# Optimization experiments

Measured on AMD Instinct MI355X. Metric: run time of the kernel, lower is better.

The kernel has to match this reference:

```python
import jax, jax.numpy as jnp
import numpy as np

N_NODES = 50000
N_EDGES = 800000
D_IN = 128
D_OUT = 128


def setup_inputs() -> dict:
    key = jax.random.key(0)
    k1, k2, k3, k4, k5 = jax.random.split(key, 5)
    x = jax.random.normal(k1, (N_NODES, D_IN), dtype=jnp.float32)
    edge_index = jax.random.randint(k2, (2, N_EDGES), 0, N_NODES, dtype=jnp.int64)
    scale = 1.0 / np.sqrt(D_IN)
    W_rel = jax.random.normal(k3, (D_OUT, D_IN), dtype=jnp.float32) * scale
    b_rel = jax.random.normal(k4, (D_OUT,), dtype=jnp.float32) * scale
    W_root = jax.random.normal(k5, (D_OUT, D_IN), dtype=jnp.float32) * scale
    return {"x": x, "edge_index": edge_index, "W_rel": W_rel, "b_rel": b_rel, "W_root": W_root}


def reference(x, edge_index, W_rel, b_rel, W_root):
    # PyG GraphConv (aggr='add'):
    #   out_i = W_rel @ (sum_{j->i} x_j) + b_rel + W_root @ x_i
    # followed by ReLU (normalization=None, dropout=0 -> identity).
    src = edge_index[0]  # message source j
    dst = edge_index[1]  # message target i
    n = x.shape[0]
    agg = jax.ops.segment_sum(x[src], dst, num_segments=n)  # [N, D_IN]
    out = agg @ W_rel.T + b_rel + x @ W_root.T              # [N, D_OUT]
    return jax.nn.relu(out)
```

## Files before the change

kernel.cpp:

```cpp
#include <hip/hip_runtime.h>
#include <hip/hip_bf16.h>


#define N_NODES 50000
#define N_EDGES 800000
#define D 128
#define SLOTS 48
#define NPB 32
#define KC 32
#define SROW 136

#define CVT_N  (N_NODES * (D / 2))
#define PACK_N (8 * 8 * 64 * 8)

typedef __attribute__((ext_vector_type(8))) short short8;
typedef __attribute__((ext_vector_type(4))) float floatx4;

__device__ __forceinline__ float bf2f(unsigned short u) {
    return __uint_as_float((unsigned int)u << 16);
}
__device__ __forceinline__ unsigned short f2bf(float f) {
    __hip_bfloat16 h = __float2bfloat16(f);
    return *(unsigned short*)&h;
}

__device__ __forceinline__ int wave_detect_i64(const int* __restrict__ ei) {
    int lane = threadIdx.x & 63;
    int v = ei[2 * lane + 1];
    return __ballot(v == 0) == ~0ull;
}

__global__ __launch_bounds__(256) void zero_f4_kernel(float4* __restrict__ p, int n4) {
    int i = blockIdx.x * 256 + threadIdx.x;
    if (i < n4) p[i] = make_float4(0.f, 0.f, 0.f, 0.f);
}

__global__ void detect_kernel(const int* __restrict__ ei, int* __restrict__ flag) {
    if (threadIdx.x == 0 && blockIdx.x == 0) {
        int any = 0;
        for (int i = 0; i < 64; ++i) any |= ei[2 * i + 1];
        flag[0] = (any == 0) ? 1 : 0;
    }
}

__global__ __launch_bounds__(256) void prep_kernel(const float2* __restrict__ x2,
                                                   ushort2* __restrict__ xb2,
                                                   const float* __restrict__ Wrel,
                                                   const float* __restrict__ Wroot,
                                                   unsigned short* __restrict__ pwc,
                                                   int* __restrict__ cnt) {
    int i = blockIdx.x * 256 + threadIdx.x;
    if (i < CVT_N) {
        float2 f = x2[i];
        xb2[i] = make_ushort2(f2bf(f.x), f2bf(f.y));
    } else if (i < CVT_N + PACK_N) {
        int idx  = i - CVT_N;
        int j    = idx & 7;
        int lane = (idx >> 3) & 63;
        int n0   = (idx >> 9) & 7;
        int t    = idx >> 12;
        int n = n0 * 16 + (lane & 15);
        int k = t * 32 + (lane >> 4) * 8 + j;
        float w = (k < D) ? Wrel[n * D + k] : Wroot[n * D + (k - D)];
        pwc[idx] = f2bf(w);
    } else if (i < CVT_N + PACK_N + N_NODES + 4) {
        cnt[i - CVT_N - PACK_N] = 0;
    }
}

__global__ __launch_bounds__(256) void append_kernel(const int* __restrict__ ei,
                                                     int* __restrict__ cnt,
                                                     int* __restrict__ slots,
                                                     int* __restrict__ ovf_cnt,
                                                     int* __restrict__ ovf) {
    int i64 = wave_detect_i64(ei);
    int base = (blockIdx.x * 256 + threadIdx.x) * 4;
    if (base >= N_EDGES) return;
    int s0, s1, s2, s3, d0, d1, d2, d3;
    if (i64) {
        int4 a = *(const int4*)&ei[2 * base];
        int4 b = *(const int4*)&ei[2 * base + 4];
        s0 = a.x; s1 = a.z; s2 = b.x; s3 = b.z;
        int4 c = *(const int4*)&ei[2 * N_EDGES + 2 * base];
        int4 e = *(const int4*)&ei[2 * N_EDGES + 2 * base + 4];
        d0 = c.x; d1 = c.z; d2 = e.x; d3 = e.z;
    } else {
        int4 sv = *(const int4*)&ei[base];
        int4 dv = *(const int4*)&ei[N_EDGES + base];
        s0 = sv.x; s1 = sv.y; s2 = sv.z; s3 = sv.w;
        d0 = dv.x; d1 = dv.y; d2 = dv.z; d3 = dv.w;
    }
    bool v0 = (unsigned)s0 < N_NODES && (unsigned)d0 < N_NODES;
    bool v1 = (unsigned)s1 < N_NODES && (unsigned)d1 < N_NODES;
    bool v2 = (unsigned)s2 < N_NODES && (unsigned)d2 < N_NODES;
    bool v3 = (unsigned)s3 < N_NODES && (unsigned)d3 < N_NODES;
    int p0 = v0 ? atomicAdd(&cnt[d0], 1) : 0;
    int p1 = v1 ? atomicAdd(&cnt[d1], 1) : 0;
    int p2 = v2 ? atomicAdd(&cnt[d2], 1) : 0;
    int p3 = v3 ? atomicAdd(&cnt[d3], 1) : 0;
    if (v0) { if (p0 < SLOTS) slots[d0 * SLOTS + p0] = s0;
              else { int o = atomicAdd(ovf_cnt, 1); ovf[2 * o] = d0; ovf[2 * o + 1] = s0; } }
    if (v1) { if (p1 < SLOTS) slots[d1 * SLOTS + p1] = s1;
              else { int o = atomicAdd(ovf_cnt, 1); ovf[2 * o] = d1; ovf[2 * o + 1] = s1; } }
    if (v2) { if (p2 < SLOTS) slots[d2 * SLOTS + p2] = s2;
              else { int o = atomicAdd(ovf_cnt, 1); ovf[2 * o] = d2; ovf[2 * o + 1] = s2; } }
    if (v3) { if (p3 < SLOTS) slots[d3 * SLOTS + p3] = s3;
              else { int o = atomicAdd(ovf_cnt, 1); ovf[2 * o] = d3; ovf[2 * o + 1] = s3; } }
}

__global__ __launch_bounds__(256) void GraphConvLayer_55783035240593_kernel(
        const ushort2* __restrict__ xb2,
        const unsigned short* __restrict__ xb,
        const int* __restrict__ cnt,
        const int* __restrict__ slots,
        const int* __restrict__ ovf_cnt,
        const int* __restrict__ ovf,
        const unsigned short* __restrict__ pwc,
        const float* __restrict__ b_rel,
        float* __restrict__ out) {
    __shared__ unsigned short sA[16 * SROW];
    int wid  = threadIdx.x >> 6;
    int lane = threadIdx.x & 63;
    int node0 = blockIdx.x * 16;
    int tov = ovf_cnt[0];

    for (int li = 0; li < 4; ++li) {
        int node = node0 + wid * 4 + li;
        int kk = cnt[node];
        if (kk > SLOTS) kk = SLOTS;
        int myidx = (lane < kk) ? slots[node * SLOTS + lane] : 0;
        float ax = 0.f, ay = 0.f;
        for (int j = 0; j < kk; j += 8) {
            int s0 = __shfl(myidx, j);
            int s1 = __shfl(myidx, j + 1);
            int s2 = __shfl(myidx, j + 2);
            int s3 = __shfl(myidx, j + 3);
            int s4 = __shfl(myidx, j + 4);
            int s5 = __shfl(myidx, j + 5);
            int s6 = __shfl(myidx, j + 6);
            int s7 = __shfl(myidx, j + 7);
            ushort2 u0 = xb2[(size_t)s0 * (D / 2) + lane];
            ushort2 u1 = xb2[(size_t)s1 * (D / 2) + lane];
            ushort2 u2 = xb2[(size_t)s2 * (D / 2) + lane];
            ushort2 u3 = xb2[(size_t)s3 * (D / 2) + lane];
            ushort2 u4 = xb2[(size_t)s4 * (D / 2) + lane];
            ushort2 u5 = xb2[(size_t)s5 * (D / 2) + lane];
            ushort2 u6 = xb2[(size_t)s6 * (D / 2) + lane];
            ushort2 u7 = xb2[(size_t)s7 * (D / 2) + lane];
            float m1 = (j + 1 < kk) ? 1.f : 0.f;
            float m2 = (j + 2 < kk) ? 1.f : 0.f;
            float m3 = (j + 3 < kk) ? 1.f : 0.f;
            float m4 = (j + 4 < kk) ? 1.f : 0.f;
            float m5 = (j + 5 < kk) ? 1.f : 0.f;
            float m6 = (j + 6 < kk) ? 1.f : 0.f;
            float m7 = (j + 7 < kk) ? 1.f : 0.f;
            ax += bf2f(u0.x) + m1 * bf2f(u1.x) + m2 * bf2f(u2.x) + m3 * bf2f(u3.x)
                + m4 * bf2f(u4.x) + m5 * bf2f(u5.x) + m6 * bf2f(u6.x) + m7 * bf2f(u7.x);
            ay += bf2f(u0.y) + m1 * bf2f(u1.y) + m2 * bf2f(u2.y) + m3 * bf2f(u3.y)
                + m4 * bf2f(u4.y) + m5 * bf2f(u5.y) + m6 * bf2f(u6.y) + m7 * bf2f(u7.y);
        }
        if (tov > 0) {
            for (int t2 = 0; t2 < tov; ++t2) {
                if (ovf[2 * t2] == node) {
                    ushort2 u = xb2[(size_t)ovf[2 * t2 + 1] * (D / 2) + lane];
                    ax += bf2f(u.x);
                    ay += bf2f(u.y);
                }
            }
        }
        *(ushort2*)&sA[(wid * 4 + li) * SROW + 2 * lane] =
            make_ushort2(f2bf(ax), f2bf(ay));
    }
    __syncthreads();

    int m = lane & 15, quad = lane >> 4;
    const unsigned short* arow = &sA[m * SROW + quad * 8];
    const unsigned short* xrow = xb + (size_t)(node0 + m) * D + quad * 8;

    floatx4 acc0 = (floatx4){0.f, 0.f, 0.f, 0.f};
    floatx4 acc1 = (floatx4){0.f, 0.f, 0.f, 0.f};
#pragma unroll
    for (int t = 0; t < 8; ++t) {
        short8 afrag = (t < 4) ? *(const short8*)(arow + t * 32)
                               : *(const short8*)(xrow + (t - 4) * 32);
        const unsigned short* bb = pwc + ((size_t)(t * 8 + wid * 2) * 64 + lane) * 8;
        short8 b0 = *(const short8*)bb;
        short8 b1 = *(const short8*)(bb + 64 * 8);
        acc0 = __builtin_amdgcn_mfma_f32_16x16x32_bf16(afrag, b0, acc0, 0, 0, 0);
        acc1 = __builtin_amdgcn_mfma_f32_16x16x32_bf16(afrag, b1, acc1, 0, 0, 0);
    }

#pragma unroll
    for (int q = 0; q < 2; ++q) {
        floatx4 a = q ? acc1 : acc0;
        int n = (wid * 2 + q) * 16 + m;
        float bias = b_rel[n];
#pragma unroll
        for (int r = 0; r < 4; ++r) {
            int node = node0 + quad * 4 + r;
            out[(size_t)node * D + n] = fmaxf(a[r] + bias, 0.f);
        }
    }
}

__global__ __launch_bounds__(256) void pack_w_kernel(const float* __restrict__ W,
                                                     float* __restrict__ pw) {
    int idx = blockIdx.x * 256 + threadIdx.x;
    if (idx >= D * D) return;
    int o = idx >> 7, k = idx & 127;
    pw[k * D + o] = W[o * D + k];
}

__global__ __launch_bounds__(256) void hist_kernel(const int* __restrict__ ei,
                                                   int* __restrict__ deg) {
    int i64 = wave_detect_i64(ei);
    int base = (blockIdx.x * 256 + threadIdx.x) * 4;
    if (base >= N_EDGES) return;
    int d0, d1, d2, d3;
    if (i64) {
        int4 a = *(const int4*)&ei[2 * N_EDGES + 2 * base];
        int4 b = *(const int4*)&ei[2 * N_EDGES + 2 * base + 4];
        d0 = a.x; d1 = a.z; d2 = b.x; d3 = b.z;
    } else {
        int4 v = *(const int4*)&ei[N_EDGES + base];
        d0 = v.x; d1 = v.y; d2 = v.z; d3 = v.w;
    }
    if ((unsigned)d0 < N_NODES) atomicAdd(&deg[d0], 1);
    if ((unsigned)d1 < N_NODES) atomicAdd(&deg[d1], 1);
    if ((unsigned)d2 < N_NODES) atomicAdd(&deg[d2], 1);
    if ((unsigned)d3 < N_NODES) atomicAdd(&deg[d3], 1);
}

__device__ __forceinline__ int wave_iscan(int v, int lane) {
#pragma unroll
    for (int off = 1; off < 64; off <<= 1) {
        int u = __shfl_up(v, off, 64);
        if (lane >= off) v += u;
    }
    return v;
}

__global__ __launch_bounds__(1024) void scan_kernel(const int* __restrict__ deg,
                                                    int* __restrict__ offsets,
                                                    int* __restrict__ cursor) {
    __shared__ int wsum[16];
    __shared__ int base_s;
    int t = threadIdx.x, lane = t & 63, w = t >> 6;
    if (t == 0) { base_s = 0; offsets[0] = 0; }
    __syncthreads();
    for (int c0 = 0; c0 < N_NODES; c0 += 1024) {
        int idx = c0 + t;
        int v = (idx < N_NODES) ? deg[idx] : 0;
        int inc = wave_iscan(v, lane);
        if (lane == 63) wsum[w] = inc;
        __syncthreads();
        if (w == 0) {
            int s = (lane < 16) ? wsum[lane] : 0;
            int si = wave_iscan(s, lane);
            if (lane < 16) wsum[lane] = si - s;
        }
        __syncthreads();
        int tot = base_s + wsum[w] + inc;
        if (idx < N_NODES) {
            offsets[idx + 1] = tot;
            cursor[idx] = tot - v;
        }
        __syncthreads();
        if (t == 1023) base_s = tot;
        __syncthreads();
    }
}

__global__ __launch_bounds__(256) void reorder_kernel(const int* __restrict__ ei,
                                                      int* __restrict__ cursor,
                                                      int* __restrict__ csr_src) {
    int i64 = wave_detect_i64(ei);
    int base = (blockIdx.x * 256 + threadIdx.x) * 4;
    if (base >= N_EDGES) return;
    int s0, s1, s2, s3, d0, d1, d2, d3;
    if (i64) {
        int4 a = *(const int4*)&ei[2 * base];
        int4 b = *(const int4*)&ei[2 * base + 4];
        s0 = a.x; s1 = a.z; s2 = b.x; s3 = b.z;
        int4 c = *(const int4*)&ei[2 * N_EDGES + 2 * base];
        int4 e = *(const int4*)&ei[2 * N_EDGES + 2 * base + 4];
        d0 = c.x; d1 = c.z; d2 = e.x; d3 = e.z;
    } else {
        int4 sv = *(const int4*)&ei[base];
        int4 dv = *(const int4*)&ei[N_EDGES + base];
        s0 = sv.x; s1 = sv.y; s2 = sv.z; s3 = sv.w;
        d0 = dv.x; d1 = dv.y; d2 = dv.z; d3 = dv.w;
    }
    bool v0 = (unsigned)s0 < N_NODES && (unsigned)d0 < N_NODES;
    bool v1 = (unsigned)s1 < N_NODES && (unsigned)d1 < N_NODES;
    bool v2 = (unsigned)s2 < N_NODES && (unsigned)d2 < N_NODES;
    bool v3 = (unsigned)s3 < N_NODES && (unsigned)d3 < N_NODES;
    int p0 = v0 ? atomicAdd(&cursor[d0], 1) : 0;
    int p1 = v1 ? atomicAdd(&cursor[d1], 1) : 0;
    int p2 = v2 ? atomicAdd(&cursor[d2], 1) : 0;
    int p3 = v3 ? atomicAdd(&cursor[d3], 1) : 0;
    if (v0) csr_src[p0] = s0;
    if (v1) csr_src[p1] = s1;
    if (v2) csr_src[p2] = s2;
    if (v3) csr_src[p3] = s3;
}

__global__ __launch_bounds__(256) void gather_kernel(const float2* __restrict__ x2,
                                                     const int* __restrict__ csr_src,
                                                     const int* __restrict__ offsets,
                                                     float2* __restrict__ agg2) {
    int node = blockIdx.x * 4 + (threadIdx.x >> 6);
    int lane = threadIdx.x & 63;
    if (node >= N_NODES) return;
    int beg = offsets[node], end = offsets[node + 1];
    float2 acc = make_float2(0.f, 0.f);
    for (int e = beg; e < end; ++e) {
        int s = csr_src[e];
        float2 f = x2[(size_t)s * (D / 2) + lane];
        acc.x += f.x;
        acc.y += f.y;
    }
    agg2[(size_t)node * (D / 2) + lane] = acc;
}

__global__ __launch_bounds__(256) void scatter_kernel(const float2* __restrict__ x2,
                                                      const int* __restrict__ ei,
                                                      const int* __restrict__ flag,
                                                      float* __restrict__ agg) {
    int wave = threadIdx.x >> 6;
    int lane = threadIdx.x & 63;
    int e = blockIdx.x * 4 + wave;
    if (e >= N_EDGES) return;
    int i64 = flag ? flag[0] : 0;
    int s, d;
    if (i64) { s = ei[2 * e]; d = ei[2 * N_EDGES + 2 * e]; }
    else     { s = ei[e];     d = ei[N_EDGES + e]; }
    if ((unsigned)s >= N_NODES || (unsigned)d >= N_NODES) return;
    float2 f = x2[(size_t)s * (D / 2) + lane];
    atomicAdd(&agg[(size_t)d * D + 2 * lane + 0], f.x);
    atomicAdd(&agg[(size_t)d * D + 2 * lane + 1], f.y);
}

__global__ __launch_bounds__(256) void gemm_f32_kernel(
        const float2* __restrict__ x2,
        const float* __restrict__ pwrel,
        const float* __restrict__ pwroot,
        const float* __restrict__ b_rel,
        float* __restrict__ out) {
    __shared__ float sWrel[KC * D];
    __shared__ float sWroot[KC * D];
    __shared__ float2 sAm[NPB * (KC / 2)];
    __shared__ float2 sXm[NPB * (KC / 2)];

    int t = threadIdx.x;
    int node0 = blockIdx.x * NPB;
    int tn = t >> 5;
    int to = t & 31;

    float acc[4][4];
#pragma unroll
    for (int a = 0; a < 4; ++a)
#pragma unroll
        for (int b = 0; b < 4; ++b) acc[a][b] = 0.0f;

    for (int c = 0; c < 4; ++c) {
        __syncthreads();
#pragma unroll
        for (int r = 0; r < 4; ++r) {
            int i = r * 256 + t;
            ((float4*)sWrel)[i]  = ((const float4*)(pwrel  + c * KC * D))[i];
            ((float4*)sWroot)[i] = ((const float4*)(pwroot + c * KC * D))[i];
        }
#pragma unroll
        for (int r = 0; r < 2; ++r) {
            int i = r * 256 + t;
            int n = i >> 4, k2 = i & 15;
            int node = node0 + n;
            float2 av = make_float2(0.f, 0.f), xv = make_float2(0.f, 0.f);
            if (node < N_NODES) {
                av = ((const float2*)out)[(size_t)node * (D / 2) + c * (KC / 2) + k2];
                xv = x2[(size_t)node * (D / 2) + c * (KC / 2) + k2];
            }
            sAm[i] = av;
            sXm[i] = xv;
        }
        __syncthreads();

#pragma unroll
        for (int k2 = 0; k2 < KC / 2; ++k2) {
            float4 wr0 = *(const float4*)&sWrel[(2 * k2 + 0) * D + to * 4];
            float4 wr1 = *(const float4*)&sWrel[(2 * k2 + 1) * D + to * 4];
            float4 wt0 = *(const float4*)&sWroot[(2 * k2 + 0) * D + to * 4];
            float4 wt1 = *(const float4*)&sWroot[(2 * k2 + 1) * D + to * 4];
#pragma unroll
            for (int ni = 0; ni < 4; ++ni) {
                float2 a  = sAm[(tn * 4 + ni) * (KC / 2) + k2];
                float2 xx = sXm[(tn * 4 + ni) * (KC / 2) + k2];
                acc[ni][0] += a.x * wr0.x + a.y * wr1.x + xx.x * wt0.x + xx.y * wt1.x;
                acc[ni][1] += a.x * wr0.y + a.y * wr1.y + xx.x * wt0.y + xx.y * wt1.y;
                acc[ni][2] += a.x * wr0.z + a.y * wr1.z + xx.x * wt0.z + xx.y * wt1.z;
                acc[ni][3] += a.x * wr0.w + a.y * wr1.w + xx.x * wt0.w + xx.y * wt1.w;
            }
        }
    }

    int o0 = to * 4;
    float4 bias = *(const float4*)&b_rel[o0];
#pragma unroll
    for (int ni = 0; ni < 4; ++ni) {
        int node = node0 + tn * 4 + ni;
        if (node >= N_NODES) continue;
        float4 v;
        v.x = fmaxf(acc[ni][0] + bias.x, 0.f);
        v.y = fmaxf(acc[ni][1] + bias.y, 0.f);
        v.z = fmaxf(acc[ni][2] + bias.z, 0.f);
        v.w = fmaxf(acc[ni][3] + bias.w, 0.f);
        *(float4*)&out[(size_t)node * D + o0] = v;
    }
}

__global__ __launch_bounds__(128) void gemm_fallback_kernel(const float* __restrict__ x,
                                                            const float* __restrict__ Wrel,
                                                            const float* __restrict__ Wroot,
                                                            const float* __restrict__ b_rel,
                                                            float* __restrict__ out) {
    __shared__ float rowA[D];
    __shared__ float rowX[D];
    int node = blockIdx.x;
    int o = threadIdx.x;
    rowA[o] = out[(size_t)node * D + o];
    rowX[o] = x[(size_t)node * D + o];
    __syncthreads();
    float acc = b_rel[o];
    const float4* wr = (const float4*)&Wrel[o * D];
    const float4* wt = (const float4*)&Wroot[o * D];
#pragma unroll 8
    for (int k4 = 0; k4 < D / 4; ++k4) {
        float4 w = wr[k4], u = wt[k4];
        const float* a = &rowA[k4 * 4];
        const float* xx = &rowX[k4 * 4];
        acc += a[0] * w.x + a[1] * w.y + a[2] * w.z + a[3] * w.w
             + xx[0] * u.x + xx[1] * u.y + xx[2] * u.z + xx[3] * u.w;
    }
    __syncthreads();
    out[(size_t)node * D + o] = fmaxf(acc, 0.f);
}

extern "C" void kernel_launch(void* const* d_in, const int* in_sizes, int n_in,
                              void* d_out, int out_size, void* d_ws, size_t ws_size,
                              hipStream_t stream) {
    const float* x      = (const float*)d_in[0];
    const int*   ei     = (const int*)d_in[1];
    const float* W_rel  = (const float*)d_in[2];
    const float* b_rel  = (const float*)d_in[3];
    const float* W_root = (const float*)d_in[4];
    float*       out    = (float*)d_out;

    char* p = (char*)d_ws;
    size_t o0 = 16;
    int*            flag    = (int*)p;
    unsigned short* pwc     = (unsigned short*)(p + o0);  o0 += (size_t)PACK_N * 2;
    unsigned short* xb      = (unsigned short*)(p + o0);  o0 += (size_t)N_NODES * D * 2;
    int*            cnt     = (int*)(p + o0);             o0 += (size_t)N_NODES * 4;
    int*            ovf_cnt = (int*)(p + o0);             o0 += 16;
    int*            slots   = (int*)(p + o0);             o0 += (size_t)N_NODES * SLOTS * 4;
    int*            ovf     = (int*)(p + o0);             o0 += (size_t)N_EDGES * 8;
    const size_t need_full = o0;

    size_t m0 = 16;
    float* m_pwrel  = (float*)(p + m0);  m0 += (size_t)D * D * 4;
    float* m_pwroot = (float*)(p + m0);  m0 += (size_t)D * D * 4;
    int*   m_deg    = (int*)(p + m0);    m0 += (size_t)N_NODES * 4;
    int*   m_offs   = (int*)(p + m0);    m0 += ((size_t)N_NODES + 1) * 4 + 12;
    m0 &= ~15ull;
    int*   m_csr    = (int*)(p + m0);    m0 += (size_t)N_EDGES * 4;
    const size_t need_mid = m0;
    const size_t need_pw  = 16 + 2 * (size_t)D * D * 4;

    const int eb4 = (N_EDGES / 4 + 255) / 256;

    if (ws_size >= need_full) {
        const int prep_total = CVT_N + PACK_N + N_NODES + 4;
        prep_kernel<<<(prep_total + 255) / 256, 256, 0, stream>>>(
            (const float2*)x, (ushort2*)xb, W_rel, W_root, pwc, cnt);
        append_kernel<<<eb4, 256, 0, stream>>>(ei, cnt, slots, ovf_cnt, ovf);
        GraphConvLayer_55783035240593_kernel<<<N_NODES / 16, 256, 0, stream>>>(
            (const ushort2*)xb, xb, cnt, slots, ovf_cnt, ovf, pwc, b_rel, out);
    } else if (ws_size >= need_mid) {
        pack_w_kernel<<<64, 256, 0, stream>>>(W_rel, m_pwrel);
        pack_w_kernel<<<64, 256, 0, stream>>>(W_root, m_pwroot);
        zero_f4_kernel<<<(N_NODES / 4 + 255) / 256, 256, 0, stream>>>((float4*)m_deg,
                                                                      N_NODES / 4);
        hist_kernel<<<eb4, 256, 0, stream>>>(ei, m_deg);
        scan_kernel<<<1, 1024, 0, stream>>>(m_deg, m_offs, m_deg);
        reorder_kernel<<<eb4, 256, 0, stream>>>(ei, m_deg, m_csr);
        gather_kernel<<<N_NODES / 4, 256, 0, stream>>>((const float2*)x, m_csr,
                                                       m_offs, (float2*)out);
        gemm_f32_kernel<<<(N_NODES + NPB - 1) / NPB, 256, 0, stream>>>(
            (const float2*)x, m_pwrel, m_pwroot, b_rel, out);
    } else {
        bool have_flag = ws_size >= 16;
        bool have_pw   = ws_size >= need_pw;
        if (have_flag) detect_kernel<<<1, 64, 0, stream>>>(ei, flag);
        if (have_pw) {
            pack_w_kernel<<<64, 256, 0, stream>>>(W_rel, m_pwrel);
            pack_w_kernel<<<64, 256, 0, stream>>>(W_root, m_pwroot);
        }
        int n4 = N_NODES * D / 4;
        zero_f4_kernel<<<(n4 + 255) / 256, 256, 0, stream>>>((float4*)out, n4);
        scatter_kernel<<<N_EDGES / 4, 256, 0, stream>>>((const float2*)x, ei,
                                                        have_flag ? flag : nullptr, out);
        if (have_pw)
            gemm_f32_kernel<<<(N_NODES + NPB - 1) / NPB, 256, 0, stream>>>(
                (const float2*)x, m_pwrel, m_pwroot, b_rel, out);
        else
            gemm_fallback_kernel<<<N_NODES, 128, 0, stream>>>(x, W_rel, W_root, b_rel, out);
    }
}
```

Baseline: 179.9 us.

## Replace global per-node atomic append with two-stage LDS bucket binning

Edge bucketing now runs in two passes. Stage 1 bins edges into 782 buckets of 64 destination nodes, using LDS atomics plus one global atomic per bucket per block, and runs the bf16 conversion of x in the same launch. Stage 2 builds the per-node slot lists with LDS counters, and slot indices shrink to 16-bit with 40 slots. The aim is to remove contended global atomics and scattered writes, at the cost of an extra kernel, a memset and an intermediate bucket buffer, plus more overflow handling because of the smaller slot count.

```diff
diff --git a/kernel.cpp b/kernel.cpp
--- a/kernel.cpp
+++ b/kernel.cpp
@@ -5,7 +5,10 @@
 #define N_NODES 50000
 #define N_EDGES 800000
 #define D 128
-#define SLOTS 48
+#define SLOTS 40
+#define NB 782
+#define BCAP 1536
+#define BINB 196
 #define NPB 32
 #define KC 32
 #define SROW 136
@@ -43,76 +46,136 @@
     }
 }
 
-__global__ __launch_bounds__(256) void prep_kernel(const float2* __restrict__ x2,
-                                                   ushort2* __restrict__ xb2,
-                                                   const float* __restrict__ Wrel,
-                                                   const float* __restrict__ Wroot,
-                                                   unsigned short* __restrict__ pwc,
-                                                   int* __restrict__ cnt) {
-    int i = blockIdx.x * 256 + threadIdx.x;
-    if (i < CVT_N) {
-        float2 f = x2[i];
-        xb2[i] = make_ushort2(f2bf(f.x), f2bf(f.y));
-    } else if (i < CVT_N + PACK_N) {
-        int idx  = i - CVT_N;
-        int j    = idx & 7;
-        int lane = (idx >> 3) & 63;
-        int n0   = (idx >> 9) & 7;
-        int t    = idx >> 12;
-        int n = n0 * 16 + (lane & 15);
-        int k = t * 32 + (lane >> 4) * 8 + j;
-        float w = (k < D) ? Wrel[n * D + k] : Wroot[n * D + (k - D)];
-        pwc[idx] = f2bf(w);
-    } else if (i < CVT_N + PACK_N + N_NODES + 4) {
-        cnt[i - CVT_N - PACK_N] = 0;
-    }
-}
-
-__global__ __launch_bounds__(256) void append_kernel(const int* __restrict__ ei,
-                                                     int* __restrict__ cnt,
-                                                     int* __restrict__ slots,
+__global__ __launch_bounds__(256) void stage1_kernel(const float2* __restrict__ x2,
+                                                     ushort2* __restrict__ xb2,
+                                                     const float* __restrict__ Wrel,
+                                                     const float* __restrict__ Wroot,
+                                                     unsigned short* __restrict__ pwc,
+                                                     const int* __restrict__ ei,
+                                                     int* __restrict__ gcur,
+                                                     unsigned* __restrict__ bmem,
                                                      int* __restrict__ ovf_cnt,
                                                      int* __restrict__ ovf) {
-    int i64 = wave_detect_i64(ei);
-    int base = (blockIdx.x * 256 + threadIdx.x) * 4;
-    if (base >= N_EDGES) return;
-    int s0, s1, s2, s3, d0, d1, d2, d3;
-    if (i64) {
-        int4 a = *(const int4*)&ei[2 * base];
-        int4 b = *(const int4*)&ei[2 * base + 4];
-        s0 = a.x; s1 = a.z; s2 = b.x; s3 = b.z;
-        int4 c = *(const int4*)&ei[2 * N_EDGES + 2 * base];
-        int4 e = *(const int4*)&ei[2 * N_EDGES + 2 * base + 4];
-        d0 = c.x; d1 = c.z; d2 = e.x; d3 = e.z;
+    __shared__ int lds_cnt[NB];
+    __shared__ int lds_base[NB];
+    if (blockIdx.x < BINB) {
+        int t = threadIdx.x;
+        int i64 = wave_detect_i64(ei);
+        for (int i = t; i < NB; i += 256) lds_cnt[i] = 0;
+        __syncthreads();
+
+        unsigned rec[16];
+        int rnk[16];
+#pragma unroll
+        for (int g = 0; g < 4; ++g) {
+            int base = blockIdx.x * 4096 + g * 1024 + t * 4;
+            int s0 = -1, s1 = -1, s2 = -1, s3 = -1;
+            int d0 = -1, d1 = -1, d2 = -1, d3 = -1;
+            if (base < N_EDGES) {
+                if (i64) {
+                    int4 a = *(const int4*)&ei[2 * base];
+                    int4 b = *(const int4*)&ei[2 * base + 4];
+                    s0 = a.x; s1 = a.z; s2 = b.x; s3 = b.z;
+                    int4 c = *(const int4*)&ei[2 * N_EDGES + 2 * base];
+                    int4 e = *(const int4*)&ei[2 * N_EDGES + 2 * base + 4];
+                    d0 = c.x; d1 = c.z; d2 = e.x; d3 = e.z;
+                } else {
+                    int4 sv = *(const int4*)&ei[base];
+                    int4 dv = *(const int4*)&ei[N_EDGES + base];
+                    s0 = sv.x; s1 = sv.y; s2 = sv.z; s3 = sv.w;
+                    d0 = dv.x; d1 = dv.y; d2 = dv.z; d3 = dv.w;
+                }
+            }
+#define BINP(idx, ss, dd)                                                        \
+            {                                                                    \
+                bool ok = (unsigned)(ss) < N_NODES && (unsigned)(dd) < N_NODES;  \
+                rec[idx] = ok ? (((unsigned)(dd) << 16) | (unsigned)(ss))        \
+                              : 0xFFFFFFFFu;                                     \
+                rnk[idx] = ok ? atomicAdd(&lds_cnt[(unsigned)(dd) >> 6], 1) : 0; \
+            }
+            BINP(g * 4 + 0, s0, d0)
+            BINP(g * 4 + 1, s1, d1)
+            BINP(g * 4 + 2, s2, d2)
+            BINP(g * 4 + 3, s3, d3)
+#undef BINP
+        }
+        __syncthreads();
+        for (int i = t; i < NB; i += 256) {
+            int c = lds_cnt[i];
+            lds_base[i] = c ? atomicAdd(&gcur[i], c) : 0;
+        }
+        __syncthreads();
+#pragma unroll
+        for (int idx = 0; idx < 16; ++idx) {
+            unsigned r = rec[idx];
+            if (r != 0xFFFFFFFFu) {
+                int bk = (int)(r >> 22);
+                int pos = lds_base[bk] + rnk[idx];
+                if (pos < BCAP) {
+                    bmem[(size_t)bk * BCAP + pos] = r;
+                } else {
+                    int o = atomicAdd(ovf_cnt, 1);
+                    ovf[2 * o] = (int)(r >> 16);
+                    ovf[2 * o + 1] = (int)(r & 0xFFFFu);
+                }
+            }
+        }
     } else {
-        int4 sv = *(const int4*)&ei[base];
-        int4 dv = *(const int4*)&ei[N_EDGES + base];
-        s0 = sv.x; s1 = sv.y; s2 = sv.z; s3 = sv.w;
-        d0 = dv.x; d1 = dv.y; d2 = dv.z; d3 = dv.w;
-    }
-    bool v0 = (unsigned)s0 < N_NODES && (unsigned)d0 < N_NODES;
-    bool v1 = (unsigned)s1 < N_NODES && (unsigned)d1 < N_NODES;
-    bool v2 = (unsigned)s2 < N_NODES && (unsigned)d2 < N_NODES;
-    bool v3 = (unsigned)s3 < N_NODES && (unsigned)d3 < N_NODES;
-    int p0 = v0 ? atomicAdd(&cnt[d0], 1) : 0;
-    int p1 = v1 ? atomicAdd(&cnt[d1], 1) : 0;
-    int p2 = v2 ? atomicAdd(&cnt[d2], 1) : 0;
-    int p3 = v3 ? atomicAdd(&cnt[d3], 1) : 0;
-    if (v0) { if (p0 < SLOTS) slots[d0 * SLOTS + p0] = s0;
-              else { int o = atomicAdd(ovf_cnt, 1); ovf[2 * o] = d0; ovf[2 * o + 1] = s0; } }
-    if (v1) { if (p1 < SLOTS) slots[d1 * SLOTS + p1] = s1;
-              else { int o = atomicAdd(ovf_cnt, 1); ovf[2 * o] = d1; ovf[2 * o + 1] = s1; } }
-    if (v2) { if (p2 < SLOTS) slots[d2 * SLOTS + p2] = s2;
-              else { int o = atomicAdd(ovf_cnt, 1); ovf[2 * o] = d2; ovf[2 * o + 1] = s2; } }
-    if (v3) { if (p3 < SLOTS) slots[d3 * SLOTS + p3] = s3;
-              else { int o = atomicAdd(ovf_cnt, 1); ovf[2 * o] = d3; ovf[2 * o + 1] = s3; } }
+        int i = (blockIdx.x - BINB) * 256 + threadIdx.x;
+        if (i < CVT_N) {
+            float2 f = x2[i];
+            xb2[i] = make_ushort2(f2bf(f.x), f2bf(f.y));
+        } else if (i < CVT_N + PACK_N) {
+            int idx  = i - CVT_N;
+            int j    = idx & 7;
+            int lane = (idx >> 3) & 63;
+            int n0   = (idx >> 9) & 7;
+            int t    = idx >> 12;
+            int n = n0 * 16 + (lane & 15);
+            int k = t * 32 + (lane >> 4) * 8 + j;
+            float w = (k < D) ? Wrel[n * D + k] : Wroot[n * D + (k - D)];
+            pwc[idx] = f2bf(w);
+        }
+    }
+}
+
+__global__ __launch_bounds__(256) void stage2_kernel(const int* __restrict__ gcur,
+                                                     const unsigned* __restrict__ bmem,
+                                                     int* __restrict__ cnt,
+                                                     unsigned short* __restrict__ slots,
+                                                     int* __restrict__ ovf_cnt,
+                                                     int* __restrict__ ovf) {
+    __shared__ int lc[64];
+    int b = blockIdx.x, t = threadIdx.x;
+    if (t < 64) lc[t] = 0;
+    __syncthreads();
+    int n = gcur[b];
+    if (n > BCAP) n = BCAP;
+    for (int e = t; e < n; e += 256) {
+        unsigned r = bmem[(size_t)b * BCAP + e];
+        int d = (int)(r >> 16);
+        int s = (int)(r & 0xFFFFu);
+        int p = atomicAdd(&lc[d & 63], 1);
+        if (p < SLOTS) {
+            slots[d * SLOTS + p] = (unsigned short)s;
+        } else {
+            int o = atomicAdd(ovf_cnt, 1);
+            ovf[2 * o] = d;
+            ovf[2 * o + 1] = s;
+        }
+    }
+    __syncthreads();
+    if (t < 64) {
+        int node = b * 64 + t;
+        if (node < N_NODES) cnt[node] = lc[t];
+    }
 }
 
 __global__ __launch_bounds__(256) void GraphConvLayer_55783035240593_kernel(
         const ushort2* __restrict__ xb2,
         const unsigned short* __restrict__ xb,
         const int* __restrict__ cnt,
-        const int* __restrict__ slots,
+        const unsigned short* __restrict__ slots,
         const int* __restrict__ ovf_cnt,
         const int* __restrict__ ovf,
         const unsigned short* __restrict__ pwc,
@@ -128,7 +191,7 @@
         int node = node0 + wid * 4 + li;
         int kk = cnt[node];
         if (kk > SLOTS) kk = SLOTS;
-        int myidx = (lane < kk) ? slots[node * SLOTS + lane] : 0;
+        int myidx = (lane < kk) ? (int)slots[node * SLOTS + lane] : 0;
         float ax = 0.f, ay = 0.f;
         for (int j = 0; j < kk; j += 8) {
             int s0 = __shfl(myidx, j);
@@ -462,8 +525,11 @@
     unsigned short* pwc     = (unsigned short*)(p + o0);  o0 += (size_t)PACK_N * 2;
     unsigned short* xb      = (unsigned short*)(p + o0);  o0 += (size_t)N_NODES * D * 2;
     int*            cnt     = (int*)(p + o0);             o0 += (size_t)N_NODES * 4;
+    const size_t gcur_pad = ((size_t)NB * 4 + 15) & ~(size_t)15;
+    int*            gcur    = (int*)(p + o0);             o0 += gcur_pad;
     int*            ovf_cnt = (int*)(p + o0);             o0 += 16;
-    int*            slots   = (int*)(p + o0);             o0 += (size_t)N_NODES * SLOTS * 4;
+    unsigned short* slots   = (unsigned short*)(p + o0);  o0 += (size_t)N_NODES * SLOTS * 2;
+    unsigned*       bmem    = (unsigned*)(p + o0);        o0 += (size_t)NB * BCAP * 4;
     int*            ovf     = (int*)(p + o0);             o0 += (size_t)N_EDGES * 8;
     const size_t need_full = o0;
 
@@ -480,10 +546,13 @@
     const int eb4 = (N_EDGES / 4 + 255) / 256;
 
     if (ws_size >= need_full) {
-        const int prep_total = CVT_N + PACK_N + N_NODES + 4;
-        prep_kernel<<<(prep_total + 255) / 256, 256, 0, stream>>>(
-            (const float2*)x, (ushort2*)xb, W_rel, W_root, pwc, cnt);
-        append_kernel<<<eb4, 256, 0, stream>>>(ei, cnt, slots, ovf_cnt, ovf);
+        hipMemsetAsync(gcur, 0, gcur_pad + 16, stream);
+        const int prep_total = CVT_N + PACK_N;
+        const int grid1 = BINB + (prep_total + 255) / 256;
+        stage1_kernel<<<grid1, 256, 0, stream>>>(
+            (const float2*)x, (ushort2*)xb, W_rel, W_root, pwc, ei,
+            gcur, bmem, ovf_cnt, ovf);
+        stage2_kernel<<<NB, 256, 0, stream>>>(gcur, bmem, cnt, slots, ovf_cnt, ovf);
         GraphConvLayer_55783035240593_kernel<<<N_NODES / 16, 256, 0, stream>>>(
             (const ushort2*)xb, xb, cnt, slots, ovf_cnt, ovf, pwc, b_rel, out);
     } else if (ws_size >= need_mid) {
```

Result: faster. 148.7 us (-17.3%).
